# Performance work log

Hardware: AMD Instinct MI355X
Metric: run time of the kernel (lower is better)

The kernel has to match this reference:

```python
import jax, jax.numpy as jnp
import numpy as np

BATCH_SIZE = 512
N_PARTS = 4
TEMP_FAC = 0.1
D = 4096
EPS = 1e-6


def _static_indices():
    # bs and factor per the n_parts==4, batch_size!=12 branch
    bs = 4 * BATCH_SIZE
    factor = 10 * N_PARTS
    pos = np.arange(bs)
    active = pos[pos % (3 * N_PARTS) < N_PARTS]            # positions that contribute
    # i1..i6 = (pos + k*n_parts) % bs for k = 0..5
    I = (active[:, None] + np.arange(6)[None, :] * N_PARTS) % bs   # (P, 6)
    # denominator indices removed: (pos + k*n_parts) % bs for k = 0..factor*n_parts-1
    offs = (active[:, None] + np.arange(factor * N_PARTS)[None, :] * N_PARTS) % bs
    M = np.ones((active.shape[0], bs), dtype=np.float32)
    M[np.arange(active.shape[0])[:, None], offs] = 0.0     # (P, bs) denominator mask
    return I, M

_I, _M = _static_indices()
# symmetrical-loss pairs: (i1,i2),(i2,i3),(i1,i4),(i4,i5),(i5,i6),(i2,i5),(i3,i6)
_PAIRS = [(0, 1), (1, 2), (0, 3), (3, 4), (4, 5), (1, 4), (2, 5)]


def setup_inputs() -> dict:
    key = jax.random.key(0)
    reg_pred = jax.random.normal(key, (4 * BATCH_SIZE, D), dtype=jnp.float32)
    return {"reg_pred": reg_pred}


def reference(reg_pred):
    I = jnp.asarray(_I)
    M = jnp.asarray(_M)
    norms = jnp.linalg.norm(reg_pred, axis=1)              # (bs,)
    # torch CosineSimilarity: dot / max(||a||*||b||, eps)
    gram = reg_pred @ reg_pred.T                           # (bs, bs)
    S = gram / jnp.maximum(norms[:, None] * norms[None, :], EPS) / TEMP_FAC
    E = jnp.exp(S)                                         # (bs, bs)
    # denominator exp-sums for each anchor role k at each active position p
    Dsum = jnp.einsum('pkb,pb->pk', E[I], M)               # (P, 6)
    total = jnp.float32(0.0)
    for a, b in _PAIRS:
        num = S[I[:, a], I[:, b]]                          # (P,)
        en = jnp.exp(num)
        total = total + jnp.sum(-jnp.log(en / (en + Dsum[:, a]))
                                - jnp.log(en / (en + Dsum[:, b])))
    return total / (6 * BATCH_SIZE)
```

## Files before the change

kernel.cpp:

```cpp
#include <hip/hip_runtime.h>
#include <hip/hip_bf16.h>
#include <stdint.h>

#define NROWS 2048
#define DIM   4096
#define NACT  684
#define INV_TEMP 10.0f
#define NTILE128 136
#define KSPLIT 2
#define KSEG  2048
#define KIT   32
#define FP8_SCALE 16.0f
#define PART_SCALE (1.0f / 256.0f)

#define WAITCNT_VM0   0x0F70
#define WAITCNT_VM4   0x0F74
#define WAITCNT_VM8   0x0F78

typedef __attribute__((ext_vector_type(4))) float floatx4;
typedef __attribute__((ext_vector_type(16))) float floatx16;
typedef __attribute__((ext_vector_type(4))) int intx4;
typedef __attribute__((ext_vector_type(8))) int intx8;
typedef __attribute__((ext_vector_type(8))) short shortx8;
typedef __attribute__((ext_vector_type(8))) unsigned short ushortx8;

static __device__ __forceinline__ unsigned short f32_to_bf16(float f) {
  union { float f; unsigned int u; } v; v.f = f;
  unsigned int u = v.u;
  unsigned int r = u + 0x7fffu + ((u >> 16) & 1u);
  return (unsigned short)(r >> 16);
}
static __device__ __forceinline__ float bf16_to_f32(unsigned short u) {
  union { unsigned int u; float f; } v; v.u = ((unsigned int)u) << 16;
  return v.f;
}
static __device__ __forceinline__ unsigned short f32_to_f16(float f) {
  _Float16 h = (_Float16)f;
  union { _Float16 h; unsigned short u; } v; v.h = h;
  return v.u;
}
static __device__ __forceinline__ float f16_to_f32(unsigned short u) {
  union { unsigned short u; _Float16 h; } v; v.u = u;
  return (float)v.h;
}

static __device__ __forceinline__ void num_store(float* __restrict__ NUM, int R, int delta,
                                                 float v) {
  if (delta == 4) {
    const int qs[4]  = {0, 1, 3, 4};
    const int pas[4] = {0, 1, 3, 4};
#pragma unroll
    for (int u = 0; u < 4; u++) {
      const int aa = (R - 4 * pas[u]) & (NROWS - 1);
      if (aa % 12 < 4) NUM[((aa / 12) * 4 + (aa % 12)) * 7 + qs[u]] = v;
    }
  } else {
    const int qs[3]  = {2, 5, 6};
    const int pas[3] = {0, 1, 2};
#pragma unroll
    for (int u = 0; u < 3; u++) {
      const int aa = (R - 4 * pas[u]) & (NROWS - 1);
      if (aa % 12 < 4) NUM[((aa / 12) * 4 + (aa % 12)) * 7 + qs[u]] = v;
    }
  }
}

__global__ __launch_bounds__(256) void k_normconv_fp8(const float* __restrict__ X,
                                                      unsigned char* __restrict__ Yq,
                                                      float* __restrict__ T,
                                                      float* __restrict__ WS,
                                                      float* __restrict__ out) {
  const int row = blockIdx.x;
  if (threadIdx.x == 0) T[row] = 0.f;
  if (row == 0 && threadIdx.x == 64) *out = 0.f;
  if (row < NACT && threadIdx.x >= 192 && threadIdx.x < 198)
    WS[row * 6 + (threadIdx.x - 192)] = 0.f;
  const float4* xr = (const float4*)(X + (size_t)row * DIM);
  float4 v[4];
  float s = 0.f;
#pragma unroll
  for (int t = 0; t < 4; t++) {
    float4 w = xr[threadIdx.x + t * 256];
    v[t] = w;
    s += w.x * w.x + w.y * w.y + w.z * w.z + w.w * w.w;
  }
#pragma unroll
  for (int off = 32; off > 0; off >>= 1) s += __shfl_down(s, off, 64);
  __shared__ float wsum[4];
  if ((threadIdx.x & 63) == 0) wsum[threadIdx.x >> 6] = s;
  __syncthreads();
  const float total = wsum[0] + wsum[1] + wsum[2] + wsum[3];
  const float sc = FP8_SCALE / fmaxf(sqrtf(total), 1e-30f);
  unsigned int* yr = (unsigned int*)(Yq + (size_t)row * DIM);
#pragma unroll
  for (int t = 0; t < 4; t++) {
    float4 w = v[t];
    unsigned int r0 = __builtin_amdgcn_cvt_pk_fp8_f32(w.x * sc, w.y * sc, 0, false);
    r0 = __builtin_amdgcn_cvt_pk_fp8_f32(w.z * sc, w.w * sc, r0, true);
    yr[threadIdx.x + t * 256] = r0;
  }
}

__global__ __launch_bounds__(256) void k_gemm_mx(const unsigned char* __restrict__ Yq,
                                                 unsigned short* __restrict__ P) {
  __shared__ __attribute__((aligned(16))) unsigned char lds[3 * 16384];
  const int bid0 = blockIdx.x;
  const int bid = (bid0 & 7) * 34 + (bid0 >> 3);
  const int kz = bid & 1;
  const int t  = bid >> 1;
  int ti = 0, rem = t;
  while (rem >= 16 - ti) { rem -= 16 - ti; ti++; }
  const int tj = ti + rem;
  const int row0 = ti * 128;
  const int col0 = tj * 128;
  const int kbase = kz * KSEG;

  const int tid  = threadIdx.x;
  const int lane = tid & 63;
  const int wave = tid >> 6;
  const int wr = wave >> 1;
  const int wc = wave & 1;

  floatx16 zero = {0.f, 0.f, 0.f, 0.f, 0.f, 0.f, 0.f, 0.f,
                   0.f, 0.f, 0.f, 0.f, 0.f, 0.f, 0.f, 0.f};
  floatx16 acc[2][2];
#pragma unroll
  for (int i = 0; i < 2; i++)
#pragma unroll
    for (int j = 0; j < 2; j++) acc[i][j] = zero;

  const int r2  = tid >> 2;
  const int c16 = tid & 3;
  const unsigned int swst = (unsigned)(((r2 >> 1) & 3) << 4);
  const unsigned int colst = ((unsigned)(c16 << 4)) ^ swst;
  const unsigned char* gA = Yq + (size_t)(row0 + r2) * DIM + kbase + colst;
  const unsigned char* gB = Yq + (size_t)(col0 + r2) * DIM + kbase + colst;

#define ISSUE(st, koff)                                                                  \
  do {                                                                                   \
    __builtin_amdgcn_global_load_lds(                                                    \
        (const __attribute__((address_space(1))) void*)(gA + (koff)),                    \
        (__attribute__((address_space(3))) void*)(lds + (st) * 16384 + tid * 16),        \
        16, 0, 0);                                                                       \
    __builtin_amdgcn_global_load_lds(                                                    \
        (const __attribute__((address_space(1))) void*)(gA + (size_t)64 * DIM + (koff)), \
        (__attribute__((address_space(3))) void*)(lds + (st) * 16384 + 4096 + tid * 16), \
        16, 0, 0);                                                                       \
    __builtin_amdgcn_global_load_lds(                                                    \
        (const __attribute__((address_space(1))) void*)(gB + (koff)),                    \
        (__attribute__((address_space(3))) void*)(lds + (st) * 16384 + 8192 + tid * 16), \
        16, 0, 0);                                                                       \
    __builtin_amdgcn_global_load_lds(                                                    \
        (const __attribute__((address_space(1))) void*)(gB + (size_t)64 * DIM + (koff)), \
        (__attribute__((address_space(3))) void*)(lds + (st) * 16384 + 12288 + tid * 16),\
        16, 0, 0);                                                                       \
  } while (0)

#define COMPUTE(st)                                                                      \
  do {                                                                                   \
    const unsigned char* bA = lds + (st) * 16384;                                        \
    const unsigned char* bB = bA + 8192;                                                 \
    const unsigned int c0 = (unsigned)((lane >> 5) << 5);                                \
    intx8 af[2], bf[2];                                                                  \
    _Pragma("unroll")                                                                    \
    for (int mi = 0; mi < 2; mi++) {                                                     \
      const int r = wr * 64 + mi * 32 + (lane & 31);                                     \
      const unsigned int sw = (unsigned)(((r >> 1) & 3) << 4);                           \
      const unsigned char* base = bA + r * 64;                                           \
      intx4 lo = *(const intx4*)(base + (c0 ^ sw));                                      \
      intx4 hi = *(const intx4*)(base + ((c0 ^ sw) ^ 16u));                              \
      intx8 v;                                                                           \
      v[0] = lo[0]; v[1] = lo[1]; v[2] = lo[2]; v[3] = lo[3];                            \
      v[4] = hi[0]; v[5] = hi[1]; v[6] = hi[2]; v[7] = hi[3];                            \
      af[mi] = v;                                                                        \
    }                                                                                    \
    _Pragma("unroll")                                                                    \
    for (int ni = 0; ni < 2; ni++) {                                                     \
      const int r = wc * 64 + ni * 32 + (lane & 31);                                     \
      const unsigned int sw = (unsigned)(((r >> 1) & 3) << 4);                           \
      const unsigned char* base = bB + r * 64;                                           \
      intx4 lo = *(const intx4*)(base + (c0 ^ sw));                                      \
      intx4 hi = *(const intx4*)(base + ((c0 ^ sw) ^ 16u));                              \
      intx8 v;                                                                           \
      v[0] = lo[0]; v[1] = lo[1]; v[2] = lo[2]; v[3] = lo[3];                            \
      v[4] = hi[0]; v[5] = hi[1]; v[6] = hi[2]; v[7] = hi[3];                            \
      bf[ni] = v;                                                                        \
    }                                                                                    \
    _Pragma("unroll")                                                                    \
    for (int mi = 0; mi < 2; mi++)                                                       \
      _Pragma("unroll")                                                                  \
      for (int ni = 0; ni < 2; ni++)                                                     \
        acc[mi][ni] = __builtin_amdgcn_mfma_scale_f32_32x32x64_f8f6f4(                   \
            af[mi], bf[ni], acc[mi][ni], 0, 0, 0, 0x7F7F7F7F, 0, 0x7F7F7F7F);            \
  } while (0)

  ISSUE(0, 0);
  ISSUE(1, 64);
#pragma unroll
  for (int k = 0; k < KIT; k++) {
    const int cur = k % 3;
    if (k < KIT - 2) {
      ISSUE((k + 2) % 3, (k + 2) * 64);
      __builtin_amdgcn_s_waitcnt(WAITCNT_VM8);
    } else if (k == KIT - 2) {
      __builtin_amdgcn_s_waitcnt(WAITCNT_VM4);
    } else {
      __builtin_amdgcn_s_waitcnt(WAITCNT_VM0);
    }
    __builtin_amdgcn_sched_barrier(0);
    __builtin_amdgcn_s_barrier();
    COMPUTE(cur);
    if (k < KIT - 1) {
      __builtin_amdgcn_s_barrier();
      __builtin_amdgcn_sched_barrier(0);
    }
  }

#undef ISSUE
#undef COMPUTE

  unsigned short* dst = P + (size_t)(t * KSPLIT + kz) * 16384;
  const int cc = lane & 31;
  const int cr = (lane >> 5) * 4;
#pragma unroll
  for (int mi = 0; mi < 2; mi++) {
#pragma unroll
    for (int ni = 0; ni < 2; ni++) {
      const int col = wc * 64 + ni * 32 + cc;
#pragma unroll
      for (int q = 0; q < 4; q++) {
        const int row = wr * 64 + mi * 32 + q * 8 + cr;
        unsigned int d0 = (unsigned int)f32_to_bf16(acc[mi][ni][q * 4 + 0] * PART_SCALE) |
                          ((unsigned int)f32_to_bf16(acc[mi][ni][q * 4 + 1] * PART_SCALE) << 16);
        unsigned int d1 = (unsigned int)f32_to_bf16(acc[mi][ni][q * 4 + 2] * PART_SCALE) |
                          ((unsigned int)f32_to_bf16(acc[mi][ni][q * 4 + 3] * PART_SCALE) << 16);
        uint2 v; v.x = d0; v.y = d1;
        *(uint2*)(dst + (size_t)col * 128 + row) = v;
      }
    }
  }
}

__global__ __launch_bounds__(512) void k_combine_full(const unsigned short* __restrict__ P,
                                                      float* __restrict__ T,
                                                      float* __restrict__ WS,
                                                      float* __restrict__ NUM) {
  __shared__ float tileE[128 * 129];
  __shared__ float colpart[128];
  const int t = blockIdx.x;
  int ti = 0, rem = t;
  while (rem >= 16 - ti) { rem -= 16 - ti; ti++; }
  const int tj = ti + rem;
  const int gr = ti * 128, gc = tj * 128;
  const int tid = threadIdx.x;
  const int c = tid >> 2;
  const int q = tid & 3;

  float evsum = 0.f;
  {
    const ushortx8* p0 = (const ushortx8*)(P + (size_t)(t * KSPLIT + 0) * 16384 +
                                           (size_t)c * 128 + q * 32);
    const ushortx8* p1 = (const ushortx8*)(P + (size_t)(t * KSPLIT + 1) * 16384 +
                                           (size_t)c * 128 + q * 32);
#pragma unroll
    for (int b = 0; b < 4; b++) {
      ushortx8 u0 = p0[b];
      ushortx8 u1 = p1[b];
#pragma unroll
      for (int e = 0; e < 8; e++) {
        const int r = q * 32 + b * 8 + e;
        const float v = (bf16_to_f32((unsigned short)u0[e]) +
                         bf16_to_f32((unsigned short)u1[e])) * INV_TEMP;
        const float ev = __expf(v);
        tileE[r * 129 + c] = ev;
        evsum += ev;
        const int D = (gc + c - gr - r) & (NROWS - 1);
        if (D == 4 || D == 12) num_store(NUM, gr + r, D, v);
        if (ti != tj && (D == 2044 || D == 2036)) num_store(NUM, gc + c, 2048 - D, v);
      }
    }
  }
  evsum += __shfl_xor(evsum, 1, 64);
  evsum += __shfl_xor(evsum, 2, 64);
  if (q == 0) colpart[c] = evsum;
  __syncthreads();

  if (tid < 128) {
    const int R = gr + tid;
#pragma unroll
    for (int k = 0; k < 6; k++) {
      const int aa = (R - 4 * k) & (NROWS - 1);
      if (aa % 12 < 4) {
        const int p2 = (aa / 12) * 4 + (aa % 12);
        const int csel = aa & 3;
        const int j0 = ((gc >> 2) - (aa >> 2)) & 511;
        float w = 0.f;
#pragma unroll
        for (int i2 = 0; i2 < 32; i2++) {
          const int j = j0 + i2;
          if (j < 160 || j >= 512) w += tileE[tid * 129 + 4 * i2 + csel];
        }
        atomicAdd(&WS[p2 * 6 + k], w);
      }
    }
  } else if (tid < 256) {
    if (ti != tj) {
      const int col = tid - 128;
      const int R = gc + col;
#pragma unroll
      for (int k = 0; k < 6; k++) {
        const int aa = (R - 4 * k) & (NROWS - 1);
        if (aa % 12 < 4) {
          const int p2 = (aa / 12) * 4 + (aa % 12);
          const int csel = aa & 3;
          const int j0 = ((gr >> 2) - (aa >> 2)) & 511;
          float w = 0.f;
#pragma unroll
          for (int i2 = 0; i2 < 32; i2++) {
            const int j = j0 + i2;
            if (j < 160 || j >= 512) w += tileE[(4 * i2 + csel) * 129 + col];
          }
          atomicAdd(&WS[p2 * 6 + k], w);
        }
      }
    }
  } else if (tid < 384) {
    if (ti != tj) {
      const int r = tid - 256;
      float rs = 0.f;
#pragma unroll 8
      for (int cc2 = 0; cc2 < 128; cc2++) rs += tileE[r * 129 + cc2];
      atomicAdd(&T[gr + r], rs);
    }
  } else {
    const int cc2 = tid - 384;
    atomicAdd(&T[gc + cc2], colpart[cc2]);
  }
}

__global__ __launch_bounds__(256) void k_finalA(const float* __restrict__ NUM,
                                                const float* __restrict__ WS,
                                                const float* __restrict__ T,
                                                float* __restrict__ out) {
  const int pa[7] = {0, 1, 0, 3, 4, 1, 2};
  const int pb[7] = {1, 2, 3, 4, 5, 4, 5};
  const int idx = blockIdx.x * 256 + threadIdx.x;
  float s = 0.f;
  if (idx < NACT * 7) {
    const int p = idx / 7;
    const int q = idx - p * 7;
    const int a0 = 12 * (p >> 2) + (p & 3);
    const int ra = (a0 + 4 * pa[q]) & (NROWS - 1);
    const int rb = (a0 + 4 * pb[q]) & (NROWS - 1);
    const float dsA = T[ra] - WS[p * 6 + pa[q]];
    const float dsB = T[rb] - WS[p * 6 + pb[q]];
    const float num = NUM[idx];
    const float en = __expf(num);
    s = __logf(en + dsA) + __logf(en + dsB) - 2.f * num;
  }
#pragma unroll
  for (int off = 32; off > 0; off >>= 1) s += __shfl_down(s, off, 64);
  if ((threadIdx.x & 63) == 0) atomicAdd(out, s * (1.0f / (6.0f * 512.0f)));
}

__global__ __launch_bounds__(256) void k_normconv(const float* __restrict__ X,
                                                  unsigned short* __restrict__ Y) {
  const int row = blockIdx.x;
  const float4* xr = (const float4*)(X + (size_t)row * DIM);
  float4 v[4];
  float s = 0.f;
#pragma unroll
  for (int t = 0; t < 4; t++) {
    float4 w = xr[threadIdx.x + t * 256];
    v[t] = w;
    s += w.x * w.x + w.y * w.y + w.z * w.z + w.w * w.w;
  }
#pragma unroll
  for (int off = 32; off > 0; off >>= 1) s += __shfl_down(s, off, 64);
  __shared__ float wsum[4];
  if ((threadIdx.x & 63) == 0) wsum[threadIdx.x >> 6] = s;
  __syncthreads();
  const float total = wsum[0] + wsum[1] + wsum[2] + wsum[3];
  const float inv = 1.0f / fmaxf(sqrtf(total), 1e-30f);
  ushort4* yr = (ushort4*)(Y + (size_t)row * DIM);
#pragma unroll
  for (int t = 0; t < 4; t++) {
    float4 w = v[t];
    ushort4 o;
    o.x = f32_to_bf16(w.x * inv);
    o.y = f32_to_bf16(w.y * inv);
    o.z = f32_to_bf16(w.z * inv);
    o.w = f32_to_bf16(w.w * inv);
    yr[threadIdx.x + t * 256] = o;
  }
}

__global__ __launch_bounds__(256) void k_gemm(const unsigned short* __restrict__ Y,
                                              float* __restrict__ S) {
  __shared__ __attribute__((aligned(16))) unsigned short sA[128 * 32];
  __shared__ __attribute__((aligned(16))) unsigned short sB[128 * 32];
  const int tid  = threadIdx.x;
  const int lane = tid & 63;
  const int wave = tid >> 6;
  const int wr = wave >> 1;
  const int wc = wave & 1;
  const int row0 = blockIdx.y * 128;
  const int col0 = blockIdx.x * 128;

  floatx4 zero = {0.f, 0.f, 0.f, 0.f};
  floatx4 acc[4][4];
#pragma unroll
  for (int i = 0; i < 4; i++)
#pragma unroll
    for (int j = 0; j < 4; j++) acc[i][j] = zero;

  const int sr = tid >> 2;
  const int sc = (tid & 3) * 8;
  const unsigned short* gA0 = Y + (size_t)(row0 + sr) * DIM + sc;
  const unsigned short* gA1 = gA0 + (size_t)64 * DIM;
  const unsigned short* gB0 = Y + (size_t)(col0 + sr) * DIM + sc;
  const unsigned short* gB1 = gB0 + (size_t)64 * DIM;

  const int fr = lane & 15;
  const int fc = (lane >> 4) * 8;

  for (int k0 = 0; k0 < DIM; k0 += 32) {
    __builtin_amdgcn_global_load_lds(
        (const __attribute__((address_space(1))) void*)(gA0 + k0),
        (__attribute__((address_space(3))) void*)(sA + tid * 8), 16, 0, 0);
    __builtin_amdgcn_global_load_lds(
        (const __attribute__((address_space(1))) void*)(gA1 + k0),
        (__attribute__((address_space(3))) void*)(sA + 2048 + tid * 8), 16, 0, 0);
    __builtin_amdgcn_global_load_lds(
        (const __attribute__((address_space(1))) void*)(gB0 + k0),
        (__attribute__((address_space(3))) void*)(sB + tid * 8), 16, 0, 0);
    __builtin_amdgcn_global_load_lds(
        (const __attribute__((address_space(1))) void*)(gB1 + k0),
        (__attribute__((address_space(3))) void*)(sB + 2048 + tid * 8), 16, 0, 0);
    __syncthreads();

    shortx8 af[4], bf[4];
#pragma unroll
    for (int mi = 0; mi < 4; mi++)
      af[mi] = *(const shortx8*)(sA + (wr * 64 + mi * 16 + fr) * 32 + fc);
#pragma unroll
    for (int ni = 0; ni < 4; ni++)
      bf[ni] = *(const shortx8*)(sB + (wc * 64 + ni * 16 + fr) * 32 + fc);
#pragma unroll
    for (int mi = 0; mi < 4; mi++)
#pragma unroll
      for (int ni = 0; ni < 4; ni++)
        acc[mi][ni] = __builtin_amdgcn_mfma_f32_16x16x32_bf16(af[mi], bf[ni], acc[mi][ni], 0, 0, 0);
    __syncthreads();
  }

  const int cc  = lane & 15;
  const int cr4 = (lane >> 4) * 4;
#pragma unroll
  for (int mi = 0; mi < 4; mi++) {
    const int row = row0 + wr * 64 + mi * 16 + cr4;
#pragma unroll
    for (int ni = 0; ni < 4; ni++) {
      const int col = col0 + wc * 64 + ni * 16 + cc;
      float* dst = S + (size_t)row * NROWS + col;
#pragma unroll
      for (int r = 0; r < 4; r++) dst[(size_t)r * NROWS] = acc[mi][ni][r] * INV_TEMP;
    }
  }
}

__global__ __launch_bounds__(256) void k_rowsum(const float* __restrict__ S,
                                                float* __restrict__ T) {
  const int row = blockIdx.x;
  const float* sr = S + (size_t)row * NROWS;
  float s = 0.f;
  for (int b = threadIdx.x; b < NROWS; b += 256) s += __expf(sr[b]);
#pragma unroll
  for (int off = 32; off > 0; off >>= 1) s += __shfl_down(s, off, 64);
  __shared__ float wsum[4];
  if ((threadIdx.x & 63) == 0) wsum[threadIdx.x >> 6] = s;
  __syncthreads();
  if (threadIdx.x == 0) T[row] = wsum[0] + wsum[1] + wsum[2] + wsum[3];
}

__global__ __launch_bounds__(64) void k_dsum(const float* __restrict__ S,
                                             const float* __restrict__ T,
                                             float* __restrict__ Ds) {
  const int p = blockIdx.x;
  const int k = blockIdx.y;
  const int a = 12 * (p >> 2) + (p & 3);
  const int lane = threadIdx.x;
  const int row = (a + 4 * k) & (NROWS - 1);
  const int m = a >> 2;
  const int c = a & 3;
  const float4* sr4 = (const float4*)(S + (size_t)row * NROWS);
  float s = 0.f;
  {
    float4 v0 = sr4[(m + lane) & 511];
    float4 v1 = sr4[(m + 64 + lane) & 511];
    float e0 = c == 0 ? v0.x : c == 1 ? v0.y : c == 2 ? v0.z : v0.w;
    float e1 = c == 0 ? v1.x : c == 1 ? v1.y : c == 2 ? v1.z : v1.w;
    s += __expf(e0) + __expf(e1);
    if (lane < 32) {
      float4 v2 = sr4[(m + 128 + lane) & 511];
      float e2 = c == 0 ? v2.x : c == 1 ? v2.y : c == 2 ? v2.z : v2.w;
      s += __expf(e2);
    }
  }
#pragma unroll
  for (int off = 32; off > 0; off >>= 1) s += __shfl_down(s, off, 64);
  if (lane == 0) Ds[p * 6 + k] = T[row] - s;
}

__global__ __launch_bounds__(256) void k_final(const float* __restrict__ S,
                                               const float* __restrict__ Ds,
                                               float* __restrict__ out) {
  const int pa[7] = {0, 1, 0, 3, 4, 1, 2};
  const int pb[7] = {1, 2, 3, 4, 5, 4, 5};
  const int idx = blockIdx.x * 256 + threadIdx.x;
  float s = 0.f;
  if (idx < NACT * 7) {
    const int p = idx / 7;
    const int q = idx - p * 7;
    const int a0 = 12 * (p >> 2) + (p & 3);
    const int ra = (a0 + 4 * pa[q]) & (NROWS - 1);
    const int rb = (a0 + 4 * pb[q]) & (NROWS - 1);
    const float num = S[(size_t)ra * NROWS + rb];
    const float en = __expf(num);
    s = __logf(en + Ds[p * 6 + pa[q]]) + __logf(en + Ds[p * 6 + pb[q]]) - 2.f * num;
  }
#pragma unroll
  for (int off = 32; off > 0; off >>= 1) s += __shfl_down(s, off, 64);
  if ((threadIdx.x & 63) == 0) atomicAdd(out, s * (1.0f / (6.0f * 512.0f)));
}

extern "C" void kernel_launch(void* const* d_in, const int* in_sizes, int n_in,
                              void* d_out, int out_size, void* d_ws, size_t ws_size,
                              hipStream_t stream) {
  const float* X = (const float*)d_in[0];
  char* ws = (char*)d_ws;
  float* out = (float*)d_out;

  const size_t pOff = (size_t)32 * 1024 * 1024;
  const size_t pBytes = (size_t)NTILE128 * KSPLIT * 16384 * 2;
  const size_t needA = pOff + 8192 + 24576 + 24576;

  if (ws_size >= needA) {
    unsigned char* Yq = (unsigned char*)ws;
    unsigned short* P = (unsigned short*)(ws + (size_t)16 * 1024 * 1024);
    float* T   = (float*)(ws + pOff);
    float* WS  = (float*)(ws + pOff + 8192);
    float* NUM = (float*)(ws + pOff + 8192 + 24576);
    (void)pBytes;
    hipLaunchKernelGGL(k_normconv_fp8, dim3(NROWS), dim3(256), 0, stream, X, Yq, T, WS, out);
    hipLaunchKernelGGL(k_gemm_mx, dim3(NTILE128 * KSPLIT), dim3(256), 0, stream, Yq, P);
    hipLaunchKernelGGL(k_combine_full, dim3(NTILE128), dim3(512), 0, stream, P, T, WS, NUM);
    hipLaunchKernelGGL(k_finalA, dim3((NACT * 7 + 255) / 256), dim3(256), 0, stream,
                       NUM, WS, T, out);
  } else {
    unsigned short* Y = (unsigned short*)ws;
    float* S = (float*)(ws + (size_t)16 * 1024 * 1024);
    float* T  = (float*)(ws + pOff);
    float* Ds = (float*)(ws + pOff + 8192);
    hipMemsetAsync(out, 0, sizeof(float), stream);
    hipLaunchKernelGGL(k_normconv, dim3(NROWS), dim3(256), 0, stream, X, Y);
    hipLaunchKernelGGL(k_gemm, dim3(16, 16), dim3(256), 0, stream, Y, S);
    hipLaunchKernelGGL(k_rowsum, dim3(NROWS), dim3(256), 0, stream, S, T);
    hipLaunchKernelGGL(k_dsum, dim3(NACT, 6), dim3(64), 0, stream, S, T, Ds);
    hipLaunchKernelGGL(k_final, dim3((NACT * 7 + 255) / 256), dim3(256), 0, stream, S, Ds, out);
  }
}
```

Baseline: 113.6 us.

## Fuse combine epilogue into FP8 GEMM and drop split-K partials

```diff
diff --git a/kernel.cpp b/kernel.cpp
--- a/kernel.cpp
+++ b/kernel.cpp
@@ -7,11 +7,9 @@
 #define NACT  684
 #define INV_TEMP 10.0f
 #define NTILE128 136
-#define KSPLIT 2
-#define KSEG  2048
-#define KIT   32
+#define KIT   64
 #define FP8_SCALE 16.0f
-#define PART_SCALE (1.0f / 256.0f)
+#define OUT_SCALE (INV_TEMP / 256.0f)
 
 #define WAITCNT_VM0   0x0F70
 #define WAITCNT_VM4   0x0F74
@@ -33,11 +31,6 @@
 static __device__ __forceinline__ float bf16_to_f32(unsigned short u) {
   union { unsigned int u; float f; } v; v.u = ((unsigned int)u) << 16;
   return v.f;
-}
-static __device__ __forceinline__ unsigned short f32_to_f16(float f) {
-  _Float16 h = (_Float16)f;
-  union { _Float16 h; unsigned short u; } v; v.h = h;
-  return v.u;
 }
 static __device__ __forceinline__ float f16_to_f32(unsigned short u) {
   union { unsigned short u; _Float16 h; } v; v.u = u;
@@ -101,19 +94,18 @@
   }
 }
 
-__global__ __launch_bounds__(256) void k_gemm_mx(const unsigned char* __restrict__ Yq,
-                                                 unsigned short* __restrict__ P) {
-  __shared__ __attribute__((aligned(16))) unsigned char lds[3 * 16384];
+__global__ __launch_bounds__(256) void k_gemm_full(const unsigned char* __restrict__ Yq,
+                                                   float* __restrict__ T,
+                                                   float* __restrict__ WS,
+                                                   float* __restrict__ NUM) {
+  __shared__ __attribute__((aligned(16))) unsigned char lds[67072];
   const int bid0 = blockIdx.x;
-  const int bid = (bid0 & 7) * 34 + (bid0 >> 3);
-  const int kz = bid & 1;
-  const int t  = bid >> 1;
+  const int t = (bid0 & 7) * 17 + (bid0 >> 3);
   int ti = 0, rem = t;
   while (rem >= 16 - ti) { rem -= 16 - ti; ti++; }
   const int tj = ti + rem;
-  const int row0 = ti * 128;
-  const int col0 = tj * 128;
-  const int kbase = kz * KSEG;
+  const int gr = ti * 128;
+  const int gc = tj * 128;
 
   const int tid  = threadIdx.x;
   const int lane = tid & 63;
@@ -133,8 +125,8 @@
   const int c16 = tid & 3;
   const unsigned int swst = (unsigned)(((r2 >> 1) & 3) << 4);
   const unsigned int colst = ((unsigned)(c16 << 4)) ^ swst;
-  const unsigned char* gA = Yq + (size_t)(row0 + r2) * DIM + kbase + colst;
-  const unsigned char* gB = Yq + (size_t)(col0 + r2) * DIM + kbase + colst;
+  const unsigned char* gA = Yq + (size_t)(gr + r2) * DIM + colst;
+  const unsigned char* gB = Yq + (size_t)(gc + r2) * DIM + colst;
 
 #define ISSUE(st, koff)                                                                  \
   do {                                                                                   \
@@ -219,70 +211,36 @@
 #undef ISSUE
 #undef COMPUTE
 
-  unsigned short* dst = P + (size_t)(t * KSPLIT + kz) * 16384;
-  const int cc = lane & 31;
-  const int cr = (lane >> 5) * 4;
-#pragma unroll
-  for (int mi = 0; mi < 2; mi++) {
-#pragma unroll
-    for (int ni = 0; ni < 2; ni++) {
-      const int col = wc * 64 + ni * 32 + cc;
-#pragma unroll
-      for (int q = 0; q < 4; q++) {
-        const int row = wr * 64 + mi * 32 + q * 8 + cr;
-        unsigned int d0 = (unsigned int)f32_to_bf16(acc[mi][ni][q * 4 + 0] * PART_SCALE) |
-                          ((unsigned int)f32_to_bf16(acc[mi][ni][q * 4 + 1] * PART_SCALE) << 16);
-        unsigned int d1 = (unsigned int)f32_to_bf16(acc[mi][ni][q * 4 + 2] * PART_SCALE) |
-                          ((unsigned int)f32_to_bf16(acc[mi][ni][q * 4 + 3] * PART_SCALE) << 16);
-        uint2 v; v.x = d0; v.y = d1;
-        *(uint2*)(dst + (size_t)col * 128 + row) = v;
+  float* tileE   = (float*)lds;
+  float* colpart = (float*)(lds + 66048);
+  __syncthreads();
+
+  {
+    float ev0 = 0.f, ev1 = 0.f;
+#pragma unroll
+    for (int mi = 0; mi < 2; mi++)
+#pragma unroll
+      for (int ni = 0; ni < 2; ni++) {
+        const int col = wc * 64 + ni * 32 + (lane & 31);
+#pragma unroll
+        for (int i = 0; i < 16; i++) {
+          const int row = wr * 64 + mi * 32 + (i & 3) + 8 * (i >> 2) + 4 * (lane >> 5);
+          const float v = acc[mi][ni][i] * OUT_SCALE;
+          const float ev = __expf(v);
+          tileE[row * 129 + col] = ev;
+          if (ni == 0) ev0 += ev; else ev1 += ev;
+          const int D = (gc + col - gr - row) & (NROWS - 1);
+          if (D == 4 || D == 12) num_store(NUM, gr + row, D, v);
+          if (ti != tj && (D == 2044 || D == 2036)) num_store(NUM, gc + col, 2048 - D, v);
+        }
       }
-    }
-  }
-}
-
-__global__ __launch_bounds__(512) void k_combine_full(const unsigned short* __restrict__ P,
-                                                      float* __restrict__ T,
-                                                      float* __restrict__ WS,
-                                                      float* __restrict__ NUM) {
-  __shared__ float tileE[128 * 129];
-  __shared__ float colpart[128];
-  const int t = blockIdx.x;
-  int ti = 0, rem = t;
-  while (rem >= 16 - ti) { rem -= 16 - ti; ti++; }
-  const int tj = ti + rem;
-  const int gr = ti * 128, gc = tj * 128;
-  const int tid = threadIdx.x;
-  const int c = tid >> 2;
-  const int q = tid & 3;
-
-  float evsum = 0.f;
-  {
-    const ushortx8* p0 = (const ushortx8*)(P + (size_t)(t * KSPLIT + 0) * 16384 +
-                                           (size_t)c * 128 + q * 32);
-    const ushortx8* p1 = (const ushortx8*)(P + (size_t)(t * KSPLIT + 1) * 16384 +
-                                           (size_t)c * 128 + q * 32);
-#pragma unroll
-    for (int b = 0; b < 4; b++) {
-      ushortx8 u0 = p0[b];
-      ushortx8 u1 = p1[b];
-#pragma unroll
-      for (int e = 0; e < 8; e++) {
-        const int r = q * 32 + b * 8 + e;
-        const float v = (bf16_to_f32((unsigned short)u0[e]) +
-                         bf16_to_f32((unsigned short)u1[e])) * INV_TEMP;
-        const float ev = __expf(v);
-        tileE[r * 129 + c] = ev;
-        evsum += ev;
-        const int D = (gc + c - gr - r) & (NROWS - 1);
-        if (D == 4 || D == 12) num_store(NUM, gr + r, D, v);
-        if (ti != tj && (D == 2044 || D == 2036)) num_store(NUM, gc + c, 2048 - D, v);
-      }
-    }
-  }
-  evsum += __shfl_xor(evsum, 1, 64);
-  evsum += __shfl_xor(evsum, 2, 64);
-  if (q == 0) colpart[c] = evsum;
+    ev0 += __shfl_xor(ev0, 32, 64);
+    ev1 += __shfl_xor(ev1, 32, 64);
+    if (lane < 32) {
+      colpart[wr * 128 + wc * 64 + (lane & 31)] = ev0;
+      colpart[wr * 128 + wc * 64 + 32 + (lane & 31)] = ev1;
+    }
+  }
   __syncthreads();
 
   if (tid < 128) {
@@ -303,38 +261,37 @@
         atomicAdd(&WS[p2 * 6 + k], w);
       }
     }
-  } else if (tid < 256) {
+  } else if (ti != tj) {
+    const int col = tid - 128;
+    const int R = gc + col;
+#pragma unroll
+    for (int k = 0; k < 6; k++) {
+      const int aa = (R - 4 * k) & (NROWS - 1);
+      if (aa % 12 < 4) {
+        const int p2 = (aa / 12) * 4 + (aa % 12);
+        const int csel = aa & 3;
+        const int j0 = ((gr >> 2) - (aa >> 2)) & 511;
+        float w = 0.f;
+#pragma unroll
+        for (int i2 = 0; i2 < 32; i2++) {
+          const int j = j0 + i2;
+          if (j < 160 || j >= 512) w += tileE[(4 * i2 + csel) * 129 + col];
+        }
+        atomicAdd(&WS[p2 * 6 + k], w);
+      }
+    }
+  }
+
+  if (tid < 128) {
     if (ti != tj) {
-      const int col = tid - 128;
-      const int R = gc + col;
-#pragma unroll
-      for (int k = 0; k < 6; k++) {
-        const int aa = (R - 4 * k) & (NROWS - 1);
-        if (aa % 12 < 4) {
-          const int p2 = (aa / 12) * 4 + (aa % 12);
-          const int csel = aa & 3;
-          const int j0 = ((gr >> 2) - (aa >> 2)) & 511;
-          float w = 0.f;
-#pragma unroll
-          for (int i2 = 0; i2 < 32; i2++) {
-            const int j = j0 + i2;
-            if (j < 160 || j >= 512) w += tileE[(4 * i2 + csel) * 129 + col];
-          }
-          atomicAdd(&WS[p2 * 6 + k], w);
-        }
-      }
-    }
-  } else if (tid < 384) {
-    if (ti != tj) {
-      const int r = tid - 256;
       float rs = 0.f;
 #pragma unroll 8
-      for (int cc2 = 0; cc2 < 128; cc2++) rs += tileE[r * 129 + cc2];
-      atomicAdd(&T[gr + r], rs);
+      for (int c2 = 0; c2 < 128; c2++) rs += tileE[tid * 129 + c2];
+      atomicAdd(&T[gr + tid], rs);
     }
   } else {
-    const int cc2 = tid - 384;
-    atomicAdd(&T[gc + cc2], colpart[cc2]);
+    const int c2 = tid - 128;
+    atomicAdd(&T[gc + c2], colpart[c2] + colpart[128 + c2]);
   }
 }
 
@@ -542,19 +499,15 @@
   float* out = (float*)d_out;
 
   const size_t pOff = (size_t)32 * 1024 * 1024;
-  const size_t pBytes = (size_t)NTILE128 * KSPLIT * 16384 * 2;
   const size_t needA = pOff + 8192 + 24576 + 24576;
 
   if (ws_size >= needA) {
     unsigned char* Yq = (unsigned char*)ws;
-    unsigned short* P = (unsigned short*)(ws + (size_t)16 * 1024 * 1024);
     float* T   = (float*)(ws + pOff);
     float* WS  = (float*)(ws + pOff + 8192);
     float* NUM = (float*)(ws + pOff + 8192 + 24576);
-    (void)pBytes;
     hipLaunchKernelGGL(k_normconv_fp8, dim3(NROWS), dim3(256), 0, stream, X, Yq, T, WS, out);
-    hipLaunchKernelGGL(k_gemm_mx, dim3(NTILE128 * KSPLIT), dim3(256), 0, stream, Yq, P);
-    hipLaunchKernelGGL(k_combine_full, dim3(NTILE128), dim3(512), 0, stream, P, T, WS, NUM);
+    hipLaunchKernelGGL(k_gemm_full, dim3(NTILE128), dim3(256), 0, stream, Yq, T, WS, NUM);
     hipLaunchKernelGGL(k_finalA, dim3((NACT * 7 + 255) / 256), dim3(256), 0, stream,
                        NUM, WS, T, out);
   } else {
```

Result: slower. 266.7 us (+134.7%).

## Split combine kernel into column-quarter blocks for more parallelism

Applied to the files above, without the earlier changes.

```diff
diff --git a/kernel.cpp b/kernel.cpp
--- a/kernel.cpp
+++ b/kernel.cpp
@@ -33,11 +33,6 @@
 static __device__ __forceinline__ float bf16_to_f32(unsigned short u) {
   union { unsigned int u; float f; } v; v.u = ((unsigned int)u) << 16;
   return v.f;
-}
-static __device__ __forceinline__ unsigned short f32_to_f16(float f) {
-  _Float16 h = (_Float16)f;
-  union { _Float16 h; unsigned short u; } v; v.h = h;
-  return v.u;
 }
 static __device__ __forceinline__ float f16_to_f32(unsigned short u) {
   union { unsigned short u; _Float16 h; } v; v.u = u;
@@ -241,49 +236,62 @@
   }
 }
 
-__global__ __launch_bounds__(512) void k_combine_full(const unsigned short* __restrict__ P,
-                                                      float* __restrict__ T,
-                                                      float* __restrict__ WS,
-                                                      float* __restrict__ NUM) {
-  __shared__ float tileE[128 * 129];
-  __shared__ float colpart[128];
+__global__ __launch_bounds__(256) void k_combine_q(const unsigned short* __restrict__ P,
+                                                   float* __restrict__ T,
+                                                   float* __restrict__ WS,
+                                                   float* __restrict__ NUM) {
+  __shared__ float tileE[32 * 132];
   const int t = blockIdx.x;
+  const int h = blockIdx.y;
   int ti = 0, rem = t;
   while (rem >= 16 - ti) { rem -= 16 - ti; ti++; }
   const int tj = ti + rem;
   const int gr = ti * 128, gc = tj * 128;
+  const int c0 = h * 32;
   const int tid = threadIdx.x;
-  const int c = tid >> 2;
-  const int q = tid & 3;
-
-  float evsum = 0.f;
+  const int cl = tid >> 3;
+  const int q  = tid & 7;
+
+  float cs = 0.f;
   {
     const ushortx8* p0 = (const ushortx8*)(P + (size_t)(t * KSPLIT + 0) * 16384 +
-                                           (size_t)c * 128 + q * 32);
+                                           (size_t)(c0 + cl) * 128 + q * 16);
     const ushortx8* p1 = (const ushortx8*)(P + (size_t)(t * KSPLIT + 1) * 16384 +
-                                           (size_t)c * 128 + q * 32);
-#pragma unroll
-    for (int b = 0; b < 4; b++) {
-      ushortx8 u0 = p0[b];
-      ushortx8 u1 = p1[b];
+                                           (size_t)(c0 + cl) * 128 + q * 16);
+    const int colg = gc + c0 + cl;
+#pragma unroll
+    for (int c2 = 0; c2 < 2; c2++) {
+      ushortx8 u0 = p0[c2];
+      ushortx8 u1 = p1[c2];
 #pragma unroll
       for (int e = 0; e < 8; e++) {
-        const int r = q * 32 + b * 8 + e;
+        const int r = q * 16 + c2 * 8 + e;
         const float v = (bf16_to_f32((unsigned short)u0[e]) +
                          bf16_to_f32((unsigned short)u1[e])) * INV_TEMP;
         const float ev = __expf(v);
-        tileE[r * 129 + c] = ev;
-        evsum += ev;
-        const int D = (gc + c - gr - r) & (NROWS - 1);
+        tileE[cl * 132 + r] = ev;
+        cs += ev;
+        const int D = (colg - gr - r) & (NROWS - 1);
         if (D == 4 || D == 12) num_store(NUM, gr + r, D, v);
-        if (ti != tj && (D == 2044 || D == 2036)) num_store(NUM, gc + c, 2048 - D, v);
+        if (ti != tj && (D == 2044 || D == 2036)) num_store(NUM, colg, 2048 - D, v);
       }
     }
   }
-  evsum += __shfl_xor(evsum, 1, 64);
-  evsum += __shfl_xor(evsum, 2, 64);
-  if (q == 0) colpart[c] = evsum;
+  cs += __shfl_xor(cs, 1, 64);
+  cs += __shfl_xor(cs, 2, 64);
+  cs += __shfl_xor(cs, 4, 64);
+  if (q == 0) atomicAdd(&T[gc + c0 + cl], cs);
   __syncthreads();
+
+  if (ti != tj) {
+    const int r = tid >> 1;
+    const int hh = tid & 1;
+    float rs = 0.f;
+#pragma unroll
+    for (int e = 0; e < 16; e++) rs += tileE[(hh * 16 + e) * 132 + r];
+    rs += __shfl_xor(rs, 1, 64);
+    if (hh == 0) atomicAdd(&T[gr + r], rs);
+  }
 
   if (tid < 128) {
     const int R = gr + tid;
@@ -293,48 +301,35 @@
       if (aa % 12 < 4) {
         const int p2 = (aa / 12) * 4 + (aa % 12);
         const int csel = aa & 3;
-        const int j0 = ((gc >> 2) - (aa >> 2)) & 511;
+        const int j0 = (((gc + c0) >> 2) - (aa >> 2)) & 511;
         float w = 0.f;
 #pragma unroll
-        for (int i2 = 0; i2 < 32; i2++) {
+        for (int i2 = 0; i2 < 8; i2++) {
           const int j = j0 + i2;
-          if (j < 160 || j >= 512) w += tileE[tid * 129 + 4 * i2 + csel];
+          if (j < 160 || j >= 512) w += tileE[(4 * i2 + csel) * 132 + tid];
         }
         atomicAdd(&WS[p2 * 6 + k], w);
       }
     }
-  } else if (tid < 256) {
-    if (ti != tj) {
-      const int col = tid - 128;
-      const int R = gc + col;
-#pragma unroll
-      for (int k = 0; k < 6; k++) {
-        const int aa = (R - 4 * k) & (NROWS - 1);
-        if (aa % 12 < 4) {
-          const int p2 = (aa / 12) * 4 + (aa % 12);
-          const int csel = aa & 3;
-          const int j0 = ((gr >> 2) - (aa >> 2)) & 511;
-          float w = 0.f;
-#pragma unroll
-          for (int i2 = 0; i2 < 32; i2++) {
-            const int j = j0 + i2;
-            if (j < 160 || j >= 512) w += tileE[(4 * i2 + csel) * 129 + col];
-          }
-          atomicAdd(&WS[p2 * 6 + k], w);
+  } else if (tid < 160 && ti != tj) {
+    const int cl2 = tid - 128;
+    const int R = gc + c0 + cl2;
+#pragma unroll
+    for (int k = 0; k < 6; k++) {
+      const int aa = (R - 4 * k) & (NROWS - 1);
+      if (aa % 12 < 4) {
+        const int p2 = (aa / 12) * 4 + (aa % 12);
+        const int csel = aa & 3;
+        const int j0 = ((gr >> 2) - (aa >> 2)) & 511;
+        float w = 0.f;
+#pragma unroll
+        for (int i2 = 0; i2 < 32; i2++) {
+          const int j = j0 + i2;
+          if (j < 160 || j >= 512) w += tileE[cl2 * 132 + 4 * i2 + csel];
         }
+        atomicAdd(&WS[p2 * 6 + k], w);
       }
     }
-  } else if (tid < 384) {
-    if (ti != tj) {
-      const int r = tid - 256;
-      float rs = 0.f;
-#pragma unroll 8
-      for (int cc2 = 0; cc2 < 128; cc2++) rs += tileE[r * 129 + cc2];
-      atomicAdd(&T[gr + r], rs);
-    }
-  } else {
-    const int cc2 = tid - 384;
-    atomicAdd(&T[gc + cc2], colpart[cc2]);
   }
 }
 
@@ -542,7 +537,6 @@
   float* out = (float*)d_out;
 
   const size_t pOff = (size_t)32 * 1024 * 1024;
-  const size_t pBytes = (size_t)NTILE128 * KSPLIT * 16384 * 2;
   const size_t needA = pOff + 8192 + 24576 + 24576;
 
   if (ws_size >= needA) {
@@ -551,10 +545,9 @@
     float* T   = (float*)(ws + pOff);
     float* WS  = (float*)(ws + pOff + 8192);
     float* NUM = (float*)(ws + pOff + 8192 + 24576);
-    (void)pBytes;
     hipLaunchKernelGGL(k_normconv_fp8, dim3(NROWS), dim3(256), 0, stream, X, Yq, T, WS, out);
     hipLaunchKernelGGL(k_gemm_mx, dim3(NTILE128 * KSPLIT), dim3(256), 0, stream, Yq, P);
-    hipLaunchKernelGGL(k_combine_full, dim3(NTILE128), dim3(512), 0, stream, P, T, WS, NUM);
+    hipLaunchKernelGGL(k_combine_q, dim3(NTILE128, 4), dim3(256), 0, stream, P, T, WS, NUM);
     hipLaunchKernelGGL(k_finalA, dim3((NACT * 7 + 255) / 256), dim3(256), 0, stream,
                        NUM, WS, T, out);
   } else {
```

Result: faster. 107.5 us (-5.4%).
